# Performance work log

Hardware: AMD Instinct MI355X
Metric: run time of the kernel (lower is better)

## Reference

```python
import jax, jax.numpy as jnp
import numpy as np

D = 1024
H = 16
HD = D // H
EPS = 1e-6


def rms_norm(x, w):
    # x: [..., hd]; compute in float32 like the torch module
    xf = x.astype(jnp.float32)
    rms = jnp.sqrt(jnp.mean(xf * xf, axis=-1, keepdims=True) + EPS)
    return (xf / rms * w.astype(jnp.float32)).astype(x.dtype)


def setup_inputs() -> dict:
    key = jax.random.key(0)
    ks = jax.random.split(key, 6)
    B, S = 2, 2048
    x = jax.random.normal(ks[0], (B, S, D), dtype=jnp.float32)
    Wqkv = jax.random.normal(ks[1], (3 * D, D), dtype=jnp.float32) * (1.0 / np.sqrt(D))
    bqkv = jax.random.normal(ks[2], (3 * D,), dtype=jnp.float32) * 0.02
    Wproj = jax.random.normal(ks[3], (D, D), dtype=jnp.float32) * (1.0 / np.sqrt(D))
    bproj = jax.random.normal(ks[4], (D,), dtype=jnp.float32) * 0.02
    qn_w = jnp.ones((HD,), dtype=jnp.float32)
    kn_w = jnp.ones((HD,), dtype=jnp.float32)
    return {"x": x, "Wqkv": Wqkv, "bqkv": bqkv, "Wproj": Wproj, "bproj": bproj,
            "qn_w": qn_w, "kn_w": kn_w}


def reference(x, Wqkv, bqkv, Wproj, bproj, qn_w, kn_w):
    B, S, _ = x.shape
    # QKV projection: torch Linear is x @ W.T + b
    qkv = x @ Wqkv.T + bqkv                     # [B, S, 3D]
    qkv = qkv.reshape(B, S, 3, H, HD)
    q, k, v = qkv[:, :, 0], qkv[:, :, 1], qkv[:, :, 2]   # each [B, S, H, hd]
    q = rms_norm(q, qn_w)
    k = rms_norm(k, kn_w)
    # move heads forward: [B, H, S, hd]
    q = q.transpose(0, 2, 1, 3)
    k = k.transpose(0, 2, 1, 3)
    v = v.transpose(0, 2, 1, 3)
    scale = 1.0 / np.sqrt(HD)
    scores = jnp.einsum('bhsd,bhtd->bhst', q, k) * scale   # [B, H, S, S] (math backend)
    attn = jax.nn.softmax(scores, axis=-1)
    out = jnp.einsum('bhst,bhtd->bhsd', attn, v)            # [B, H, S, hd]
    out = out.transpose(0, 2, 1, 3).reshape(B, S, D)
    return out @ Wproj.T + bproj
```

## Files before the change

kernel.cpp:

```cpp
#include <hip/hip_runtime.h>
#include <hip/hip_bf16.h>
#include <math.h>

#define D_MODEL 1024
#define NH 16
#define HD 64
#define SEQ 2048
#define BATCH 2
#define NTOK (BATCH*SEQ)

typedef short bf16x8 __attribute__((ext_vector_type(8)));
typedef short s4 __attribute__((ext_vector_type(4)));
typedef float f32x4 __attribute__((ext_vector_type(4)));
typedef unsigned short us4 __attribute__((ext_vector_type(4)));

#define MFMA(a,b,c) __builtin_amdgcn_mfma_f32_16x16x32_bf16(a,b,c,0,0,0)

union bfu { __hip_bfloat16 b; unsigned short u; };
__device__ __forceinline__ unsigned short f2b(float f){ bfu t; t.b = __float2bfloat16(f); return t.u; }
__device__ __forceinline__ float b2f(unsigned short u){ bfu t; t.u = u; return __bfloat162float(t.b); }
__device__ __forceinline__ unsigned short f2bf(float f){
    unsigned int u = __float_as_uint(f);
    u += 0x7FFFu + ((u >> 16) & 1u);
    return (unsigned short)(u >> 16);
}

__device__ __forceinline__ void g2l16(const unsigned short* g, unsigned short* l){
    __builtin_amdgcn_global_load_lds(
        (const __attribute__((address_space(1))) unsigned int*)g,
        (__attribute__((address_space(3))) unsigned int*)l, 16, 0, 0);
}

#define WAITVM(N) asm volatile("s_waitcnt vmcnt(" #N ")" ::: "memory")
#define RBAR do{ __builtin_amdgcn_s_barrier(); __builtin_amdgcn_sched_barrier(0); }while(0)

#define OFF_X   128L
#define OFF_WQ  (OFF_X  + 4194304L)
#define OFF_BQ  (OFF_WQ + 3145728L)
#define OFF_WP  (OFF_BQ + 3072L)
#define OFF_BP  (OFF_WP + 1048576L)
#define OFF_QN  (OFF_BP + 1024L)
#define OFF_KN  (OFF_QN + 64L)
#define OFF_Q   (OFF_KN + 64L)
#define OFF_K   (OFF_Q  + 4194304L)
#define OFF_V   (OFF_K  + 4194304L)
#define OFF_A   (OFF_V  + 4194304L)


__global__ __launch_bounds__(256) void detect_kernel(
    const unsigned int* __restrict__ xraw, int* __restrict__ cnt)
{
    int i = blockIdx.x*256 + threadIdx.x;
    uint4 v = ((const uint4*)xraw)[i];
    unsigned int w[4] = {v.x, v.y, v.z, v.w};
    int local = 0;
    #pragma unroll
    for (int j=0;j<4;j++){
        local += ((w[j] & 0x7F80u) >= 0x4800u);
        local += (((w[j]>>16) & 0x7F80u) >= 0x4800u);
    }
    if (local) atomicAdd(cnt, local);
}

__global__ __launch_bounds__(256) void convert_kernel(
    const void* __restrict__ x,  const void* __restrict__ wq,
    const void* __restrict__ bq, const void* __restrict__ wp,
    const void* __restrict__ bp, const void* __restrict__ qn,
    const void* __restrict__ kn, unsigned short* __restrict__ ws,
    const int* __restrict__ cntp)
{
    const int flag = (*cntp > 256);
    long i = (long)blockIdx.x*blockDim.x + threadIdx.x;
    const long stride = (long)gridDim.x*blockDim.x;
    const long NCH = 2098208L;
    for (; i < NCH; i += stride){
        long j = i; const void* src; long off;
        if (j < 1048576L)                  { src = x;  off = OFF_X;  }
        else if ((j -= 1048576L) < 786432L){ src = wq; off = OFF_WQ; }
        else if ((j -= 786432L)  < 768L)   { src = bq; off = OFF_BQ; }
        else if ((j -= 768L)     < 262144L){ src = wp; off = OFF_WP; }
        else if ((j -= 262144L)  < 256L)   { src = bp; off = OFF_BP; }
        else if ((j -= 256L)     < 16L)    { src = qn; off = OFF_QN; }
        else      { j -= 16L;                src = kn; off = OFF_KN; }
        us4 o;
        if (flag){
            float4 v = ((const float4*)src)[j];
            o.x = f2b(v.x); o.y = f2b(v.y); o.z = f2b(v.z); o.w = f2b(v.w);
        } else {
            o = ((const us4*)src)[j];
        }
        *(us4*)(ws + off + j*4) = o;
    }
}

__global__ __launch_bounds__(256) void qkv_kernel(
    const unsigned short* __restrict__ x,
    const unsigned short* __restrict__ Wqkv,
    const unsigned short* __restrict__ bqkv,
    const unsigned short* __restrict__ qn_w,
    const unsigned short* __restrict__ kn_w,
    unsigned short* __restrict__ qbuf,
    unsigned short* __restrict__ kbuf,
    unsigned short* __restrict__ vbuf)
{
    __shared__ __align__(16) unsigned short tA0[128*32];
    __shared__ __align__(16) unsigned short tA1[128*32];
    __shared__ __align__(16) unsigned short tB0[128*32];
    __shared__ __align__(16) unsigned short tB1[128*32];
    const int tid  = threadIdx.x;
    const int w    = tid >> 6, lane = tid & 63, quad = lane >> 4, c = lane & 15;
    const int m0 = blockIdx.y*128, n0 = blockIdx.x*128;
    const int am = (w>>1)*64, bn = (w&1)*64;
    const int kq = quad ^ ((c>>1)&3);

    f32x4 acc[4][4];
    for (int mi=0;mi<4;mi++) for (int ni=0;ni<4;ni++) acc[mi][ni] = {0.f,0.f,0.f,0.f};

    const int i0 = tid, i1 = tid + 256;
    const int r0 = i0>>2, cc0 = (i0&3) ^ ((r0>>1)&3);
    const int r1 = i1>>2, cc1 = (i1&3) ^ ((r1>>1)&3);
    const long gaA0 = (long)(m0 + r0)*D_MODEL + cc0*8;
    const long gaA1 = (long)(m0 + r1)*D_MODEL + cc1*8;
    const long gbB0 = (long)(n0 + r0)*D_MODEL + cc0*8;
    const long gbB1 = (long)(n0 + r1)*D_MODEL + cc1*8;

#define QKV_STAGE(BUFA, BUFB, T) do{ const int kk_ = (T)*32; \
    g2l16(x    + gaA0 + kk_, BUFA + i0*8); \
    g2l16(x    + gaA1 + kk_, BUFA + i1*8); \
    g2l16(Wqkv + gbB0 + kk_, BUFB + i0*8); \
    g2l16(Wqkv + gbB1 + kk_, BUFB + i1*8); \
    __builtin_amdgcn_sched_barrier(0); }while(0)

#define QKV_COMP(BUFA, BUFB) do{ \
    bf16x8 a_[4], b_[4]; \
    _Pragma("unroll") \
    for (int mi=0;mi<4;mi++) \
        a_[mi] = *(const bf16x8*)(BUFA + ((am + mi*16 + c)*4 + kq)*8); \
    _Pragma("unroll") \
    for (int ni=0;ni<4;ni++) \
        b_[ni] = *(const bf16x8*)(BUFB + ((bn + ni*16 + c)*4 + kq)*8); \
    _Pragma("unroll") \
    for (int mi=0;mi<4;mi++) \
        _Pragma("unroll") \
        for (int ni=0;ni<4;ni++) \
            acc[mi][ni] = MFMA(a_[mi], b_[ni], acc[mi][ni]); }while(0)

    QKV_STAGE(tA0, tB0, 0);
    QKV_STAGE(tA1, tB1, 1);

    for (int t=0; t<30; t+=2){
        WAITVM(4); RBAR;
        QKV_COMP(tA0, tB0);
        RBAR;
        QKV_STAGE(tA0, tB0, t+2);
        WAITVM(4); RBAR;
        QKV_COMP(tA1, tB1);
        RBAR;
        QKV_STAGE(tA1, tB1, t+3);
    }
    WAITVM(4); RBAR;
    QKV_COMP(tA0, tB0);
    WAITVM(0); RBAR;
    QKV_COMP(tA1, tB1);
#undef QKV_STAGE
#undef QKV_COMP

    const int nw = n0 + bn, mw = m0 + am;
    const int region = nw >> 10;
    const int h      = (nw & 1023) >> 6;
    float bias[4], wn[4];
    for (int ni=0;ni<4;ni++){
        bias[ni] = b2f(bqkv[nw + ni*16 + c]);
        wn[ni]   = 1.0f;
    }
    if (region==0) for (int ni=0;ni<4;ni++) wn[ni] = b2f(qn_w[ni*16+c]) * 0.18033688f;
    if (region==1) for (int ni=0;ni<4;ni++) wn[ni] = b2f(kn_w[ni*16+c]);

    for (int mi=0;mi<4;mi++){
        for (int ni=0;ni<4;ni++)
            for (int r=0;r<4;r++) acc[mi][ni][r] += bias[ni];

        float scale_r[4];
        if (region < 2){
            for (int r=0;r<4;r++){
                float ss = 0.f;
                for (int ni=0;ni<4;ni++){ float v2 = acc[mi][ni][r]; ss += v2*v2; }
                ss += __shfl_xor(ss, 1, 64);
                ss += __shfl_xor(ss, 2, 64);
                ss += __shfl_xor(ss, 4, 64);
                ss += __shfl_xor(ss, 8, 64);
                scale_r[r] = rsqrtf(ss*(1.0f/64.0f) + 1e-6f);
            }
        } else {
            for (int r=0;r<4;r++) scale_r[r] = 1.0f;
        }

        for (int r=0;r<4;r++){
            int m = mw + mi*16 + quad*4 + r;
            int bidx = m >> 11, s = m & 2047;
            long bb = (long)(bidx*NH + h)*SEQ*HD;
            if (region == 0){
                long base = bb + (long)s*HD;
                for (int ni=0;ni<4;ni++)
                    qbuf[base + ni*16 + c] = f2bf(acc[mi][ni][r] * scale_r[r] * wn[ni]);
            } else if (region == 1){
                long tb = bb + (long)(s>>6)*4096;
                for (int ni=0;ni<4;ni++){
                    int d = ni*16 + c;
                    long idx = tb + (long)((s&63)*8 + ((d>>3) ^ (s&7)))*8 + (d&7);
                    kbuf[idx] = f2bf(acc[mi][ni][r] * scale_r[r] * wn[ni]);
                }
            } else {
                long tb = bb + (long)(s>>6)*4096;
                int ch2  = (s>>4)&3;
                int fb   = ((s>>2)&3)*4;
                int mloc = s&3;
                for (int ni=0;ni<4;ni++){
                    int d = ni*16 + c;
                    int f = fb + (((d>>1) + ch2)&3);
                    long idx = tb + (long)d*64 + f*4 + mloc;
                    vbuf[idx] = f2bf(acc[mi][ni][r]);
                }
            }
        }
    }
}

__global__ __launch_bounds__(256, 4) void attn_kernel(
    const unsigned short* __restrict__ qbuf,
    const unsigned short* __restrict__ kts,
    const unsigned short* __restrict__ vts,
    unsigned short* __restrict__ abuf)
{
    const int tid = threadIdx.x, w = tid>>6, lane = tid&63, quad = lane>>4, c = lane&15;
    const int bh = blockIdx.y, qt = blockIdx.x;
    const unsigned short* qb = qbuf + (long)bh*SEQ*HD;
    const unsigned short* kb = kts + (long)bh*SEQ*HD;
    const unsigned short* vb = vts + (long)bh*SEQ*HD;
    const int qbase = qt*64 + w*16;
    const int cq = c & 7;

    __shared__ __align__(16) unsigned short KT0[4096];
    __shared__ __align__(16) unsigned short KT1[4096];
    __shared__ __align__(16) unsigned short VT0[4096];
    __shared__ __align__(16) unsigned short VT1[4096];

    bf16x8 aq[2];
    #pragma unroll
    for (int ks=0;ks<2;ks++)
        aq[ks] = *(const bf16x8*)(qb + (long)(qbase + c)*HD + ks*32 + quad*8);

    f32x4 o[4];
    #pragma unroll
    for (int nt=0;nt<4;nt++) o[nt] = {0.f,0.f,0.f,0.f};
    f32x4 l4 = {0.f,0.f,0.f,0.f};

#define STAGE2(SRC, DST) do{ \
    g2l16((SRC) + tid*8,        DST + tid*8); \
    g2l16((SRC) + 2048 + tid*8, DST + 2048 + tid*8); }while(0)

#define ATTN_TILE(KTB, VTB) do{ \
    bf16x8 kf_[4][2]; \
    _Pragma("unroll") \
    for (int mt=0;mt<4;mt++) \
        _Pragma("unroll") \
        for (int ks=0;ks<2;ks++) \
            kf_[mt][ks] = *(const bf16x8*)(KTB + ((mt*16+c)*8 + ((ks*4+quad)^cq))*8); \
    f32x4 z4_[4]; \
    _Pragma("unroll") \
    for (int mt=0;mt<4;mt++){ \
        f32x4 t_ = {0.f,0.f,0.f,0.f}; \
        t_ = MFMA(kf_[mt][0], aq[0], t_); \
        t_ = MFMA(kf_[mt][1], aq[1], t_); \
        z4_[mt] = t_; \
    } \
    unsigned int pk_[4][2]; \
    _Pragma("unroll") \
    for (int mt=0;mt<4;mt++){ \
        float p0 = __builtin_amdgcn_exp2f(z4_[mt][0]); \
        float p1 = __builtin_amdgcn_exp2f(z4_[mt][1]); \
        float p2 = __builtin_amdgcn_exp2f(z4_[mt][2]); \
        float p3 = __builtin_amdgcn_exp2f(z4_[mt][3]); \
        l4[0] += p0; l4[1] += p1; l4[2] += p2; l4[3] += p3; \
        pk_[mt][0] = __builtin_amdgcn_perm(__float_as_uint(p1), __float_as_uint(p0), 0x07060302u); \
        pk_[mt][1] = __builtin_amdgcn_perm(__float_as_uint(p3), __float_as_uint(p2), 0x07060302u); \
    } \
    _Pragma("unroll") \
    for (int ks=0;ks<2;ks++){ \
        union { unsigned int u[4]; bf16x8 v; } pB_; \
        pB_.u[0] = pk_[2*ks][0];   pB_.u[1] = pk_[2*ks][1]; \
        pB_.u[2] = pk_[2*ks+1][0]; pB_.u[3] = pk_[2*ks+1][1]; \
        _Pragma("unroll") \
        for (int nt=0;nt<4;nt++){ \
            const int dv_ = nt*16 + c; \
            const unsigned short* vbase_ = VTB + dv_*64; \
            int flo_ = quad*4 + (((dv_>>1) + ks*2    )&3); \
            int fhi_ = quad*4 + (((dv_>>1) + ks*2 + 1)&3); \
            uint2 lo_ = *(const uint2*)(vbase_ + flo_*4); \
            uint2 hi_ = *(const uint2*)(vbase_ + fhi_*4); \
            union { unsigned int u[4]; bf16x8 v; } vv_; \
            vv_.u[0]=lo_.x; vv_.u[1]=lo_.y; vv_.u[2]=hi_.x; vv_.u[3]=hi_.y; \
            o[nt] = MFMA(vv_.v, pB_.v, o[nt]); \
        } \
    } }while(0)

    STAGE2(kb, KT0); STAGE2(vb, VT0);
    __syncthreads();

    for (int kt2=0; kt2<SEQ/64; kt2+=2){
        STAGE2(kb + (kt2+1)*4096, KT1);
        STAGE2(vb + (kt2+1)*4096, VT1);
        ATTN_TILE(KT0, VT0);
        __syncthreads();
        if (kt2+2 < SEQ/64){
            STAGE2(kb + (kt2+2)*4096, KT0);
            STAGE2(vb + (kt2+2)*4096, VT0);
        }
        ATTN_TILE(KT1, VT1);
        __syncthreads();
    }
#undef STAGE2
#undef ATTN_TILE

    float l_loc = (l4[0]+l4[1]) + (l4[2]+l4[3]);
    l_loc += __shfl_xor(l_loc, 16, 64);
    l_loc += __shfl_xor(l_loc, 32, 64);
    float inv = 1.0f / l_loc;

    const int b = bh >> 4, h = bh & 15;
    long base = ((long)(b*SEQ + qbase + c)*NH + h)*HD;
    #pragma unroll
    for (int nt=0;nt<4;nt++){
        us4 pkd;
        #pragma unroll
        for (int r=0;r<4;r++) pkd[r] = f2bf(o[nt][r]*inv);
        *(us4*)(abuf + base + nt*16 + quad*4) = pkd;
    }
}

__global__ __launch_bounds__(256) void proj_kernel(
    const unsigned short* __restrict__ abuf,
    const unsigned short* __restrict__ Wp,
    const unsigned short* __restrict__ bp,
    void* __restrict__ outv,
    const int* __restrict__ cntp)
{
    __shared__ __align__(16) unsigned short tA0[128*32];
    __shared__ __align__(16) unsigned short tA1[128*32];
    __shared__ __align__(16) unsigned short tB0[64*32];
    __shared__ __align__(16) unsigned short tB1[64*32];
    const int tid  = threadIdx.x;
    const int w    = tid >> 6, lane = tid & 63, quad = lane >> 4, c = lane & 15;
    const int m0 = blockIdx.y*128, n0 = blockIdx.x*64;
    const int am = (w>>1)*64, bn = (w&1)*32;
    const int kq = quad ^ ((c>>1)&3);
    const int flag = (*cntp > 256);

    f32x4 acc[4][2];
    for (int mi=0;mi<4;mi++) for (int ni=0;ni<2;ni++) acc[mi][ni] = {0.f,0.f,0.f,0.f};

    const int i0 = tid, i1 = tid + 256;
    const int r0 = i0>>2, cc0 = (i0&3) ^ ((r0>>1)&3);
    const int r1 = i1>>2, cc1 = (i1&3) ^ ((r1>>1)&3);
    const long gaA0 = (long)(m0 + r0)*D_MODEL + cc0*8;
    const long gaA1 = (long)(m0 + r1)*D_MODEL + cc1*8;
    const long gbB0 = (long)(n0 + r0)*D_MODEL + cc0*8;

#define PROJ_STAGE(BUFA, BUFB, T) do{ const int kk_ = (T)*32; \
    g2l16(abuf + gaA0 + kk_, BUFA + i0*8); \
    g2l16(abuf + gaA1 + kk_, BUFA + i1*8); \
    g2l16(Wp   + gbB0 + kk_, BUFB + i0*8); }while(0)

#define PROJ_COMP(BUFA, BUFB) do{ \
    bf16x8 a_[4], b_[2]; \
    _Pragma("unroll") \
    for (int mi=0;mi<4;mi++) \
        a_[mi] = *(const bf16x8*)(BUFA + ((am + mi*16 + c)*4 + kq)*8); \
    _Pragma("unroll") \
    for (int ni=0;ni<2;ni++) \
        b_[ni] = *(const bf16x8*)(BUFB + ((bn + ni*16 + c)*4 + kq)*8); \
    _Pragma("unroll") \
    for (int mi=0;mi<4;mi++) \
        _Pragma("unroll") \
        for (int ni=0;ni<2;ni++) \
            acc[mi][ni] = MFMA(a_[mi], b_[ni], acc[mi][ni]); }while(0)

    PROJ_STAGE(tA0, tB0, 0);
    __syncthreads();

    for (int t=0; t<32; t+=2){
        PROJ_STAGE(tA1, tB1, t+1);
        PROJ_COMP(tA0, tB0);
        __syncthreads();
        if (t+2 < 32) PROJ_STAGE(tA0, tB0, t+2);
        PROJ_COMP(tA1, tB1);
        __syncthreads();
    }
#undef PROJ_STAGE
#undef PROJ_COMP

    float bias[2];
    for (int ni=0;ni<2;ni++) bias[ni] = b2f(bp[n0 + bn + ni*16 + c]);

    for (int mi=0;mi<4;mi++)
        for (int r=0;r<4;r++){
            long m = m0 + am + mi*16 + quad*4 + r;
            for (int ni=0;ni<2;ni++){
                float val = acc[mi][ni][r] + bias[ni];
                long idx = m*D_MODEL + n0 + bn + ni*16 + c;
                if (flag) ((float*)outv)[idx] = val;
                else      ((unsigned short*)outv)[idx] = f2bf(val);
            }
        }
}

extern "C" void kernel_launch(void* const* d_in, const int* in_sizes, int n_in,
                              void* d_out, int out_size, void* d_ws, size_t ws_size,
                              hipStream_t stream)
{
    unsigned short* ws = (unsigned short*)d_ws;
    int* cnt = (int*)d_ws;

    hipMemsetAsync(cnt, 0, 4, stream);
    hipLaunchKernelGGL(detect_kernel, dim3(16), dim3(256), 0, stream,
                       (const unsigned int*)d_in[0], cnt);
    hipLaunchKernelGGL(convert_kernel, dim3(2048), dim3(256), 0, stream,
                       d_in[0], d_in[1], d_in[2], d_in[3], d_in[4], d_in[5], d_in[6],
                       ws, cnt);
    hipLaunchKernelGGL(qkv_kernel,  dim3(24,32), dim3(256), 0, stream,
                       ws+OFF_X, ws+OFF_WQ, ws+OFF_BQ, ws+OFF_QN, ws+OFF_KN,
                       ws+OFF_Q, ws+OFF_K, ws+OFF_V);
    hipLaunchKernelGGL(attn_kernel, dim3(32,32), dim3(256), 0, stream,
                       ws+OFF_Q, ws+OFF_K, ws+OFF_V, ws+OFF_A);
    hipLaunchKernelGGL(proj_kernel, dim3(16,32), dim3(256), 0, stream,
                       ws+OFF_A, ws+OFF_WP, ws+OFF_BP, d_out, cnt);
}
```

Before: 210.6 us.

## Pre-swizzle Wqkv into MFMA fragment layout and load B directly to registers

The convert kernel now writes Wqkv into a tiled layout matching the MFMA B-operand fragment order. The QKV GEMM then loads B fragments straight from global memory into registers with dwordx4 loads, skipping the LDS staging for B. The A pipeline becomes triple-buffered in LDS, with the B register sets rotating alongside it. This removes LDS traffic and footprint for the weight tile. In exchange it raises register pressure and relies on the hand-counted vmcnt waits being correct.

```diff
diff --git a/kernel.cpp b/kernel.cpp
--- a/kernel.cpp
+++ b/kernel.cpp
@@ -74,14 +74,18 @@
     const long stride = (long)gridDim.x*blockDim.x;
     const long NCH = 2098208L;
     for (; i < NCH; i += stride){
-        long j = i; const void* src; long off;
-        if (j < 1048576L)                  { src = x;  off = OFF_X;  }
-        else if ((j -= 1048576L) < 786432L){ src = wq; off = OFF_WQ; }
-        else if ((j -= 786432L)  < 768L)   { src = bq; off = OFF_BQ; }
-        else if ((j -= 768L)     < 262144L){ src = wp; off = OFF_WP; }
-        else if ((j -= 262144L)  < 256L)   { src = bp; off = OFF_BP; }
-        else if ((j -= 256L)     < 16L)    { src = qn; off = OFF_QN; }
-        else      { j -= 16L;                src = kn; off = OFF_KN; }
+        long j = i; const void* src; long off; long dj;
+        if (j < 1048576L)                  { src = x;  off = OFF_X;  dj = j; }
+        else if ((j -= 1048576L) < 786432L){
+            src = wq; off = OFF_WQ;
+            long n = j >> 8, k4 = j & 255;
+            dj = (n>>4)*4096 + (k4>>1)*32 + (n&15)*2 + (k4&1);
+        }
+        else if ((j -= 786432L)  < 768L)   { src = bq; off = OFF_BQ; dj = j; }
+        else if ((j -= 768L)     < 262144L){ src = wp; off = OFF_WP; dj = j; }
+        else if ((j -= 262144L)  < 256L)   { src = bp; off = OFF_BP; dj = j; }
+        else if ((j -= 256L)     < 16L)    { src = qn; off = OFF_QN; dj = j; }
+        else      { j -= 16L;                src = kn; off = OFF_KN; dj = j; }
         us4 o;
         if (flag){
             float4 v = ((const float4*)src)[j];
@@ -89,7 +93,7 @@
         } else {
             o = ((const us4*)src)[j];
         }
-        *(us4*)(ws + off + j*4) = o;
+        *(us4*)(ws + off + dj*4) = o;
     }
 }
 
@@ -105,8 +109,7 @@
 {
     __shared__ __align__(16) unsigned short tA0[128*32];
     __shared__ __align__(16) unsigned short tA1[128*32];
-    __shared__ __align__(16) unsigned short tB0[128*32];
-    __shared__ __align__(16) unsigned short tB1[128*32];
+    __shared__ __align__(16) unsigned short tA2[128*32];
     const int tid  = threadIdx.x;
     const int w    = tid >> 6, lane = tid & 63, quad = lane >> 4, c = lane & 15;
     const int m0 = blockIdx.y*128, n0 = blockIdx.x*128;
@@ -121,48 +124,69 @@
     const int r1 = i1>>2, cc1 = (i1&3) ^ ((r1>>1)&3);
     const long gaA0 = (long)(m0 + r0)*D_MODEL + cc0*8;
     const long gaA1 = (long)(m0 + r1)*D_MODEL + cc1*8;
-    const long gbB0 = (long)(n0 + r0)*D_MODEL + cc0*8;
-    const long gbB1 = (long)(n0 + r1)*D_MODEL + cc1*8;
-
-#define QKV_STAGE(BUFA, BUFB, T) do{ const int kk_ = (T)*32; \
-    g2l16(x    + gaA0 + kk_, BUFA + i0*8); \
-    g2l16(x    + gaA1 + kk_, BUFA + i1*8); \
-    g2l16(Wqkv + gbB0 + kk_, BUFB + i0*8); \
-    g2l16(Wqkv + gbB1 + kk_, BUFB + i1*8); \
+
+    const long nb16 = (long)((n0 + bn) >> 4);
+    const int  qc8  = quad*128 + c*8;
+    bf16x8 B0[4], B1[4], B2[4];
+
+#define QKV_STAGE(BUFA, T) do{ const int kk_ = (T)*32; \
+    g2l16(x + gaA0 + kk_, BUFA + i0*8); \
+    g2l16(x + gaA1 + kk_, BUFA + i1*8); \
     __builtin_amdgcn_sched_barrier(0); }while(0)
 
-#define QKV_COMP(BUFA, BUFB) do{ \
-    bf16x8 a_[4], b_[4]; \
+#define QKV_LOADB(SET, T) do{ const long kb_ = (long)(T)*512; \
+    _Pragma("unroll") \
+    for (int ni_=0;ni_<4;ni_++){ \
+        const unsigned short* p_ = Wqkv + (nb16 + ni_)*16384 + kb_ + qc8; \
+        asm volatile("global_load_dwordx4 %0, %1, off" : "=v"(SET[ni_]) : "v"(p_)); \
+    } \
+    __builtin_amdgcn_sched_barrier(0); }while(0)
+
+#define QKV_COMP(BUFA, SET) do{ \
+    bf16x8 a_[4]; \
     _Pragma("unroll") \
     for (int mi=0;mi<4;mi++) \
         a_[mi] = *(const bf16x8*)(BUFA + ((am + mi*16 + c)*4 + kq)*8); \
-    _Pragma("unroll") \
-    for (int ni=0;ni<4;ni++) \
-        b_[ni] = *(const bf16x8*)(BUFB + ((bn + ni*16 + c)*4 + kq)*8); \
     _Pragma("unroll") \
     for (int mi=0;mi<4;mi++) \
         _Pragma("unroll") \
         for (int ni=0;ni<4;ni++) \
-            acc[mi][ni] = MFMA(a_[mi], b_[ni], acc[mi][ni]); }while(0)
-
-    QKV_STAGE(tA0, tB0, 0);
-    QKV_STAGE(tA1, tB1, 1);
-
-    for (int t=0; t<30; t+=2){
-        WAITVM(4); RBAR;
-        QKV_COMP(tA0, tB0);
+            acc[mi][ni] = MFMA(a_[mi], SET[ni], acc[mi][ni]); }while(0)
+
+    QKV_STAGE(tA0, 0); QKV_LOADB(B0, 0);
+    QKV_STAGE(tA1, 1); QKV_LOADB(B1, 1);
+    QKV_STAGE(tA2, 2); QKV_LOADB(B2, 2);
+
+    for (int t=0; t<27; t+=3){
+        WAITVM(12); RBAR;
+        QKV_COMP(tA0, B0);
         RBAR;
-        QKV_STAGE(tA0, tB0, t+2);
-        WAITVM(4); RBAR;
-        QKV_COMP(tA1, tB1);
+        QKV_STAGE(tA0, t+3); QKV_LOADB(B0, t+3);
+        WAITVM(12); RBAR;
+        QKV_COMP(tA1, B1);
         RBAR;
-        QKV_STAGE(tA1, tB1, t+3);
-    }
-    WAITVM(4); RBAR;
-    QKV_COMP(tA0, tB0);
+        QKV_STAGE(tA1, t+4); QKV_LOADB(B1, t+4);
+        WAITVM(12); RBAR;
+        QKV_COMP(tA2, B2);
+        RBAR;
+        QKV_STAGE(tA2, t+5); QKV_LOADB(B2, t+5);
+    }
+    WAITVM(12); RBAR;
+    QKV_COMP(tA0, B0);
+    RBAR;
+    QKV_STAGE(tA0, 30); QKV_LOADB(B0, 30);
+    WAITVM(12); RBAR;
+    QKV_COMP(tA1, B1);
+    RBAR;
+    QKV_STAGE(tA1, 31); QKV_LOADB(B1, 31);
+    WAITVM(12); RBAR;
+    QKV_COMP(tA2, B2);
+    WAITVM(6); RBAR;
+    QKV_COMP(tA0, B0);
     WAITVM(0); RBAR;
-    QKV_COMP(tA1, tB1);
+    QKV_COMP(tA1, B1);
 #undef QKV_STAGE
+#undef QKV_LOADB
 #undef QKV_COMP
 
     const int nw = n0 + bn, mw = m0 + am;
```

After: 214.8 us. 1.02x slower.
